# Kernel tuning notes

Measured on AMD Instinct MI355X. Metric: run time of the kernel, lower is better.

Reference implementation:

```python
import jax, jax.numpy as jnp
import numpy as np

B, T, D, H = 4, 1024, 1024, 16
DH = D // H
NEG_BIG = jnp.float32(-2.0**32 + 1)


def layer_norm(x, scale, bias, eps=1e-5):
    mean = jnp.mean(x, axis=-1, keepdims=True)
    var = jnp.mean(jnp.square(x - mean), axis=-1, keepdims=True)
    return (x - mean) * jax.lax.rsqrt(var + eps) * scale + bias


def setup_inputs() -> dict:
    key = jax.random.key(0)
    ks = jax.random.split(key, 10)
    s = 0.02
    x = jax.random.normal(ks[0], (B, T, D), jnp.float32)
    mask = jax.random.randint(ks[1], (B, T), 0, 2).astype(jnp.float32)
    return {
        "x": x,
        "mask": mask,
        "wq": jax.random.normal(ks[2], (D, D), jnp.float32) * s,
        "wk": jax.random.normal(ks[3], (D, D), jnp.float32) * s,
        "wv": jax.random.normal(ks[4], (D, D), jnp.float32) * s,
        "w1": jax.random.normal(ks[5], (D, D), jnp.float32) * s,
        "b1": jnp.zeros((D,), jnp.float32),
        "w2": jax.random.normal(ks[6], (D, D), jnp.float32) * s,
        "b2": jnp.zeros((D,), jnp.float32),
        "ln1_s": jnp.ones((D,), jnp.float32),
        "ln1_b": jnp.zeros((D,), jnp.float32),
        "ln2_s": jnp.ones((D,), jnp.float32),
        "ln2_b": jnp.zeros((D,), jnp.float32),
        "ln3_s": jnp.ones((D,), jnp.float32),
        "ln3_b": jnp.zeros((D,), jnp.float32),
    }


def _mask_enc(x, mask, wq, wk, wv, w1, b1, w2, b2,
              ln1_s, ln1_b, ln2_s, ln2_b, ln3_s, ln3_b):
    b, t, d = x.shape
    # --- multi-head attention (hand-rolled, matches torch split/cat trick) ---
    Q = (x @ wq).reshape(b, t, H, DH).transpose(0, 2, 1, 3)  # [B,H,T,dh]
    K = (x @ wk).reshape(b, t, H, DH).transpose(0, 2, 1, 3)
    V = (x @ wv).reshape(b, t, H, DH).transpose(0, 2, 1, 3)
    scores = jnp.einsum('bhqd,bhkd->bhqk', Q, K) / jnp.sqrt(jnp.float32(DH))
    # key padding mask from sign of |K| row sums
    key_m = jnp.sign(jnp.sum(jnp.abs(K), axis=-1))  # [B,H,T]
    scores = jnp.where(key_m[:, :, None, :] == 0, NEG_BIG, scores)
    # FORWARD direction: allowed where col_index > row_index (strict)
    idx = jnp.arange(t)
    allowed = (idx[None, :] > idx[:, None]).astype(scores.dtype)  # [T,T]
    scores = scores + (1.0 - allowed) * (-10000.0)
    attn = jax.nn.softmax(scores, axis=-1)
    # post-softmax query mask multiply
    query_m = jnp.sign(jnp.sum(jnp.abs(Q), axis=-1))[:, :, :, None]  # [B,H,T,1]
    attn = attn * query_m
    out = jnp.einsum('bhqk,bhkd->bhqd', attn, V)
    out = out.transpose(0, 2, 1, 3).reshape(b, t, d)  # combine heads
    out = out * mask[:, :, None]
    # --- residual + layernorm wrapper (attention) ---
    h1 = layer_norm(x + out, ln1_s, ln1_b)
    # --- FFN + residual + layernorm ---
    ffn = jax.nn.relu(h1 @ w1 + b1) @ w2 + b2
    h2 = layer_norm(h1 + ffn, ln2_s, ln2_b)
    # --- output normalization ---
    return layer_norm(h2, ln3_s, ln3_b)


def reference(x, mask, wq, wk, wv, w1, b1, w2, b2,
              ln1_s, ln1_b, ln2_s, ln2_b, ln3_s, ln3_b):
    return _mask_enc(x, mask, wq, wk, wv, w1, b1, w2, b2,
                     ln1_s, ln1_b, ln2_s, ln2_b, ln3_s, ln3_b)
```

## Files before the change

### kernel.cpp

```cpp
#include <hip/hip_runtime.h>
#include <stdint.h>


#define B_  4
#define T_  1024
#define D_  1024
#define H_  16
#define DH_ 64

typedef __attribute__((ext_vector_type(8))) short short8;
typedef __attribute__((ext_vector_type(4))) float floatx4;
typedef __attribute__((ext_vector_type(4))) _Float16 half4;

__device__ __forceinline__ unsigned short f2bf(float f) {
  union { float f; uint32_t u; } a; a.f = f;
  uint32_t r = a.u + 0x7FFFu + ((a.u >> 16) & 1u);
  return (unsigned short)(r >> 16);
}
__device__ __forceinline__ float bf2f(unsigned short u) {
  union { uint32_t u; float f; } a; a.u = ((uint32_t)u) << 16;
  return a.f;
}

#define GLD_LDS16(g, l) __builtin_amdgcn_global_load_lds( \
    (const __attribute__((address_space(1))) unsigned int*)(g), \
    (__attribute__((address_space(3))) unsigned int*)(l), 16, 0, 0)

__global__ __launch_bounds__(256)
void prep_kernel(const float4* __restrict__ x4, unsigned short* __restrict__ xb,
                 const float* __restrict__ w0, const float* __restrict__ w1,
                 const float* __restrict__ w2, const float* __restrict__ w3,
                 const float* __restrict__ w4, unsigned short* __restrict__ dst_all) {
  const int t = threadIdx.x;
  if (blockIdx.x < 1024) {
    int idx0 = blockIdx.x * 1024 + t;
#pragma unroll
    for (int c = 0; c < 4; ++c) {
      int idx = idx0 + c * 256;
      float4 v = x4[idx];
      union { uint2 u; unsigned short s[4]; } o;
      o.s[0] = f2bf(v.x); o.s[1] = f2bf(v.y); o.s[2] = f2bf(v.z); o.s[3] = f2bf(v.w);
      *(uint2*)&xb[(size_t)idx * 4] = o.u;
    }
    return;
  }
  const int b = blockIdx.x - 1024;
  const int z = b >> 8, ky = (b >> 4) & 15, nx = b & 15;
  const float* src = (z == 0) ? w0 : (z == 1) ? w1 : (z == 2) ? w2 : (z == 3) ? w3 : w4;
  unsigned short* dst = dst_all + (size_t)z * D_ * D_;
  __shared__ __align__(16) unsigned short tile[64 * 72];
  const int k0 = ky * 64, n0 = nx * 64;
#pragma unroll
  for (int c = 0; c < 4; ++c) {
    int idx = c * 256 + t;
    int r = idx >> 4, cc = (idx & 15) << 2;
    float4 v = *(const float4*)&src[(size_t)(k0 + r) * D_ + n0 + cc];
    tile[(cc + 0) * 72 + r] = f2bf(v.x);
    tile[(cc + 1) * 72 + r] = f2bf(v.y);
    tile[(cc + 2) * 72 + r] = f2bf(v.z);
    tile[(cc + 3) * 72 + r] = f2bf(v.w);
  }
  __syncthreads();
  int rr = t >> 2, ck = (t & 3) << 4;
  uint4 v0 = *(const uint4*)&tile[rr * 72 + ck];
  uint4 v1 = *(const uint4*)&tile[rr * 72 + ck + 8];
  *(uint4*)&dst[(size_t)(n0 + rr) * D_ + k0 + ck] = v0;
  *(uint4*)&dst[(size_t)(n0 + rr) * D_ + k0 + ck + 8] = v1;
}

__global__ __launch_bounds__(256, 2)
void gemm_qkv(const unsigned short* __restrict__ A,
              const unsigned short* __restrict__ Bt,
              unsigned short* __restrict__ oQ, unsigned short* __restrict__ oK,
              _Float16* __restrict__ oV) {
  const int K = 1024;
  __shared__ __align__(16) unsigned short As[128 * 32];
  __shared__ __align__(16) unsigned short Bs[128 * 32];
  __shared__ __align__(16) _Float16 Cs[2 * 64 * 136];
  const int t = threadIdx.x;
  const int lane = t & 63, w = t >> 6;
  const int quad = lane >> 4, lm = lane & 15;
  const int wm = w >> 1, wn = w & 1;
  const int m0 = blockIdx.y * 128, n0 = blockIdx.x * 128;
  const int arow = w * 32 + (lane >> 2), acol = (lane & 3) << 3;

  floatx4 acc[4][4];
#pragma unroll
  for (int i = 0; i < 4; ++i)
#pragma unroll
    for (int j = 0; j < 4; ++j) acc[i][j] = (floatx4){0.f, 0.f, 0.f, 0.f};

  for (int kt = 0; kt < K; kt += 32) {
    const unsigned short* ga = A + (size_t)(m0 + arow) * K + kt + acol;
    const unsigned short* gb = Bt + (size_t)(n0 + arow) * K + kt + acol;
    GLD_LDS16(ga, &As[(w * 32) * 32]);
    GLD_LDS16(ga + (size_t)16 * K, &As[(w * 32 + 16) * 32]);
    GLD_LDS16(gb, &Bs[(w * 32) * 32]);
    GLD_LDS16(gb + (size_t)16 * K, &Bs[(w * 32 + 16) * 32]);
    __syncthreads();
    short8 a[4], b[4];
#pragma unroll
    for (int i = 0; i < 4; ++i) a[i] = *(const short8*)&As[(wm * 64 + i * 16 + lm) * 32 + quad * 8];
#pragma unroll
    for (int j = 0; j < 4; ++j) b[j] = *(const short8*)&Bs[(wn * 64 + j * 16 + lm) * 32 + quad * 8];
#pragma unroll
    for (int i = 0; i < 4; ++i)
#pragma unroll
      for (int j = 0; j < 4; ++j)
        acc[i][j] = __builtin_amdgcn_mfma_f32_16x16x32_bf16(a[i], b[j], acc[i][j], 0, 0, 0);
    __syncthreads();
  }

  if (n0 < 2048) {
    unsigned short* p = (n0 < 1024) ? oQ : oK;
    const float qscale = (n0 < 1024) ? 0.18033688f : 1.0f;
#pragma unroll
    for (int i = 0; i < 4; ++i) {
      int gmb = m0 + wm * 64 + i * 16 + quad * 4;
#pragma unroll
      for (int j = 0; j < 4; ++j) {
        int gn = n0 + wn * 64 + j * 16 + lm;
        int nn = gn & 1023, hh = nn >> 6, dd = nn & 63;
#pragma unroll
        for (int r = 0; r < 4; ++r) {
          int gm = gmb + r;
          int bb = gm >> 10, tt = gm & 1023;
          p[(((size_t)bb * H_ + hh) * T_ + tt) * DH_ + dd] = f2bf(acc[i][j][r] * qscale);
        }
      }
    }
  } else {
#pragma unroll
    for (int i = 0; i < 4; ++i) {
#pragma unroll
      for (int j = 0; j < 4; ++j) {
        int gn = n0 + wn * 64 + j * 16 + lm;
        int hd = (gn >> 6) & 1, dd = gn & 63;
        int kperm = quad * 32 + (wm * 4 + i) * 4;
        union { _Float16 h[4]; uint2 u; } pk;
#pragma unroll
        for (int r = 0; r < 4; ++r) pk.h[r] = (_Float16)acc[i][j][r];
        *(uint2*)&Cs[((size_t)(hd * 64 + dd)) * 136 + kperm] = pk.u;
      }
    }
    __syncthreads();
    const int row = t >> 1, half = t & 1;
    const int hd = row >> 6, dd = row & 63;
    const int hh = ((n0 & 1023) >> 6) + hd;
    const int bb = m0 >> 10, kbg = (m0 >> 7) & 7;
    const _Float16* srcp = &Cs[(size_t)(hd * 64 + dd) * 136 + half * 64];
    _Float16* dstp = oV + ((((size_t)bb * H_ + hh) * DH_ + dd) * 8 + kbg) * 128 + half * 64;
#pragma unroll
    for (int g = 0; g < 8; ++g)
      *(uint4*)(dstp + g * 8) = *(const uint4*)(srcp + g * 8);
  }
}

template <int MODE>
__global__ __launch_bounds__(256, 2)
void gemm_ffn(const unsigned short* __restrict__ A,
              const unsigned short* __restrict__ Bt,
              unsigned short* __restrict__ oBf,
              const float* __restrict__ bias) {
  const int K = 1024, N = 1024;
  __shared__ __align__(16) unsigned short As[64 * 32];
  __shared__ __align__(16) unsigned short Bs[128 * 32];
  const int t = threadIdx.x;
  const int lane = t & 63, w = t >> 6;
  const int quad = lane >> 4, lm = lane & 15;
  const int wm = w >> 1, wn = w & 1;
  const int m0 = blockIdx.y * 64, n0 = blockIdx.x * 128;
  const int lrow = lane >> 2, lcol = (lane & 3) << 3;

  floatx4 acc[2][4];
#pragma unroll
  for (int i = 0; i < 2; ++i)
#pragma unroll
    for (int j = 0; j < 4; ++j) acc[i][j] = (floatx4){0.f, 0.f, 0.f, 0.f};

  for (int kt = 0; kt < K; kt += 32) {
    const unsigned short* ga = A + (size_t)(m0 + w * 16 + lrow) * K + kt + lcol;
    const unsigned short* gb = Bt + (size_t)(n0 + w * 32 + lrow) * K + kt + lcol;
    GLD_LDS16(ga, &As[(w * 16) * 32]);
    GLD_LDS16(gb, &Bs[(w * 32) * 32]);
    GLD_LDS16(gb + (size_t)16 * K, &Bs[(w * 32 + 16) * 32]);
    __syncthreads();
    short8 a[2], b[4];
#pragma unroll
    for (int i = 0; i < 2; ++i) a[i] = *(const short8*)&As[(wm * 32 + i * 16 + lm) * 32 + quad * 8];
#pragma unroll
    for (int j = 0; j < 4; ++j) b[j] = *(const short8*)&Bs[(wn * 64 + j * 16 + lm) * 32 + quad * 8];
#pragma unroll
    for (int i = 0; i < 2; ++i)
#pragma unroll
      for (int j = 0; j < 4; ++j)
        acc[i][j] = __builtin_amdgcn_mfma_f32_16x16x32_bf16(a[i], b[j], acc[i][j], 0, 0, 0);
    __syncthreads();
  }

#pragma unroll
  for (int i = 0; i < 2; ++i) {
    int gmb = m0 + wm * 32 + i * 16 + quad * 4;
#pragma unroll
    for (int j = 0; j < 4; ++j) {
      int gn = n0 + wn * 64 + j * 16 + lm;
      float bv = bias[gn];
#pragma unroll
      for (int r = 0; r < 4; ++r) {
        int gm = gmb + r;
        float v = acc[i][j][r] + bv;
        if (MODE == 1) v = fmaxf(v, 0.f);
        oBf[(size_t)gm * N + gn] = f2bf(v);
      }
    }
  }
}

__global__ __launch_bounds__(256)
void flash_attn(const unsigned short* __restrict__ Qb,
                const unsigned short* __restrict__ Kb,
                const _Float16* __restrict__ Vtg,
                const float* __restrict__ maskp,
                unsigned short* __restrict__ attn) {
  __shared__ __align__(16) unsigned short KLs[2][8192];
  __shared__ __align__(16) _Float16      VLs[2][8192];

  const int t = threadIdx.x;
  const int lane = t & 63, w = t >> 6;
  const int quad = lane >> 4, lm = lane & 15;

  const int bid = blockIdx.x;
  const int hi  = bid >> 8;
  const int lo  = bid & 255;
  const int xcd = lo & 7;
  const int hgrp = (lo >> 3) & 7;
  const int qpair = lo >> 6;
  const int qb = hi ? (7 - qpair) : qpair;
  const int head = hgrp * 8 + xcd;
  const int hh = head & 15, bb = head >> 4;
  const int q0 = qb << 7;

  const size_t headoff = ((size_t)bb * H_ + hh) * T_ * DH_;
  const unsigned short* Qh = Qb + headoff;
  const unsigned short* Kh = Kb + headoff;
  const _Float16* Vh = Vtg + headoff;

  short8 qf[2][2];
#pragma unroll
  for (int qg = 0; qg < 2; ++qg)
#pragma unroll
    for (int ks = 0; ks < 2; ++ks)
      qf[qg][ks] = *(const short8*)(Qh + (size_t)(q0 + w * 32 + qg * 16 + lm) * 64 + ks * 32 + quad * 8);

  float lsum[2] = {0.f, 0.f};
  floatx4 acc[2][4];
#pragma unroll
  for (int qg = 0; qg < 2; ++qg)
#pragma unroll
    for (int j2 = 0; j2 < 4; ++j2) acc[qg][j2] = (floatx4){0.f, 0.f, 0.f, 0.f};

  const int qglob0 = q0 + w * 32 + lm;
  const bool excl1 = (qglob0 + 16 == 1023);
  const float MSHIFT = 14426.950408f;

  const int my_lo  = (qb == 7 && w == 3) ? 0 : qb;
  const int blk_lo = (qb == 7) ? 0 : qb;

  const unsigned short* gk[4];
  const _Float16* gv[4];
#pragma unroll
  for (int i = 0; i < 4; ++i) {
    int s = w * 4 + i;
    gk[i] = Kh + (size_t)((s >> 1) * 16 + lm) * 64 + (s & 1) * 32 + quad * 8;
    gv[i] = Vh + ((size_t)((s >> 2) * 16 + lm) * 8) * 128 + quad * 32 + (s & 3) * 8;
  }

#pragma unroll
  for (int i = 0; i < 4; ++i) {
    int s = w * 4 + i;
    GLD_LDS16(gk[i] + (size_t)blk_lo * 8192, &KLs[0][s * 512]);
    GLD_LDS16(gv[i] + (size_t)blk_lo * 128,  &VLs[0][s * 512]);
  }

  int cur = 0;
  for (int kb = blk_lo; kb < 8; ++kb) {
    __syncthreads();
    if (kb + 1 < 8) {
      int nxt = cur ^ 1;
#pragma unroll
      for (int i = 0; i < 4; ++i) {
        int s = w * 4 + i;
        GLD_LDS16(gk[i] + (size_t)(kb + 1) * 8192, &KLs[nxt][s * 512]);
        GLD_LDS16(gv[i] + (size_t)(kb + 1) * 128,  &VLs[nxt][s * 512]);
      }
    }
    if (kb >= my_lo) {
      const unsigned short* Kc = &KLs[cur][0];
      const _Float16* Vc = &VLs[cur][0];
      const int k0 = kb * 128;
      const bool need_mask = (kb <= qb);

      short8 kA = *(const short8*)&Kc[(0 * 64 + lane) * 8];
      short8 kB = *(const short8*)&Kc[(1 * 64 + lane) * 8];
      half4 vA0 = *(const half4*)&Vc[((0 * 4 + 0) * 64 + lane) * 8];
      half4 vA1 = *(const half4*)&Vc[((1 * 4 + 0) * 64 + lane) * 8];
      half4 vA2 = *(const half4*)&Vc[((2 * 4 + 0) * 64 + lane) * 8];
      half4 vA3 = *(const half4*)&Vc[((3 * 4 + 0) * 64 + lane) * 8];

#pragma unroll
      for (int j = 0; j < 8; ++j) {
        short8 nA, nB; half4 n0, n1, n2, n3;
        if (j < 7) {
          int jn = j + 1;
          nA = *(const short8*)&Kc[((jn * 2 + 0) * 64 + lane) * 8];
          nB = *(const short8*)&Kc[((jn * 2 + 1) * 64 + lane) * 8];
          n0 = *(const half4*)&Vc[((0 * 4 + (jn >> 1)) * 64 + lane) * 8 + (jn & 1) * 4];
          n1 = *(const half4*)&Vc[((1 * 4 + (jn >> 1)) * 64 + lane) * 8 + (jn & 1) * 4];
          n2 = *(const half4*)&Vc[((2 * 4 + (jn >> 1)) * 64 + lane) * 8 + (jn & 1) * 4];
          n3 = *(const half4*)&Vc[((3 * 4 + (jn >> 1)) * 64 + lane) * 8 + (jn & 1) * 4];
        }
        floatx4 st[2];
#pragma unroll
        for (int qg = 0; qg < 2; ++qg) {
          floatx4 z = (floatx4){0.f, 0.f, 0.f, 0.f};
          z = __builtin_amdgcn_mfma_f32_16x16x32_bf16(kA, qf[qg][0], z, 0, 0, 0);
          st[qg] = __builtin_amdgcn_mfma_f32_16x16x32_bf16(kB, qf[qg][1], z, 0, 0, 0);
        }
        half4 pa[2];
#pragma unroll
        for (int qg = 0; qg < 2; ++qg) {
          const int qq = qglob0 + qg * 16;
          const bool skip = (qg == 1) && excl1;
#pragma unroll
          for (int r = 0; r < 4; ++r) {
            int kg = k0 + j * 16 + quad * 4 + r;
            float v = st[qg][r];
            if (need_mask && !skip && kg <= qq) v -= MSHIFT;
            float p = __builtin_amdgcn_exp2f(v);
            lsum[qg] += p;
            pa[qg][r] = (_Float16)p;
          }
        }
        acc[0][0] = __builtin_amdgcn_mfma_f32_16x16x16f16(pa[0], vA0, acc[0][0], 0, 0, 0);
        acc[1][0] = __builtin_amdgcn_mfma_f32_16x16x16f16(pa[1], vA0, acc[1][0], 0, 0, 0);
        acc[0][1] = __builtin_amdgcn_mfma_f32_16x16x16f16(pa[0], vA1, acc[0][1], 0, 0, 0);
        acc[1][1] = __builtin_amdgcn_mfma_f32_16x16x16f16(pa[1], vA1, acc[1][1], 0, 0, 0);
        acc[0][2] = __builtin_amdgcn_mfma_f32_16x16x16f16(pa[0], vA2, acc[0][2], 0, 0, 0);
        acc[1][2] = __builtin_amdgcn_mfma_f32_16x16x16f16(pa[1], vA2, acc[1][2], 0, 0, 0);
        acc[0][3] = __builtin_amdgcn_mfma_f32_16x16x16f16(pa[0], vA3, acc[0][3], 0, 0, 0);
        acc[1][3] = __builtin_amdgcn_mfma_f32_16x16x16f16(pa[1], vA3, acc[1][3], 0, 0, 0);
        kA = nA; kB = nB; vA0 = n0; vA1 = n1; vA2 = n2; vA3 = n3;
      }
    }
    cur ^= 1;
  }

#pragma unroll
  for (int qg = 0; qg < 2; ++qg) {
    float l = lsum[qg];
    l += __shfl_xor(l, 16);
    l += __shfl_xor(l, 32);
    float s = maskp[bb * T_ + qglob0 + qg * 16] / l;
#pragma unroll
    for (int r = 0; r < 4; ++r) {
      float bsc = __shfl(s, quad * 4 + r);
      int tq = q0 + w * 32 + qg * 16 + quad * 4 + r;
#pragma unroll
      for (int j2 = 0; j2 < 4; ++j2)
        attn[((size_t)(bb * T_ + tq)) * D_ + hh * 64 + j2 * 16 + lm] = f2bf(acc[qg][j2][r] * bsc);
    }
  }
}

__global__ __launch_bounds__(256)
void ln_res_kernel(const float* __restrict__ xa, const unsigned short* __restrict__ attn,
                   const float* __restrict__ sc, const float* __restrict__ bi,
                   float* __restrict__ h, unsigned short* __restrict__ hb) {
  const int t = threadIdx.x;
  const int lane = t & 63, w = t >> 6;
  const int row = blockIdx.x * 4 + w;
  const size_t base = (size_t)row * D_ + lane * 16;

  float v[16];
  float s1 = 0.f, s2 = 0.f;
#pragma unroll
  for (int i = 0; i < 4; ++i) {
    float4 a = *(const float4*)&xa[base + i * 4];
    union { uint2 u; unsigned short s[4]; } au;
    au.u = *(const uint2*)&attn[base + i * 4];
    float x0 = a.x + bf2f(au.s[0]);
    float x1 = a.y + bf2f(au.s[1]);
    float x2 = a.z + bf2f(au.s[2]);
    float x3 = a.w + bf2f(au.s[3]);
    v[i * 4 + 0] = x0; v[i * 4 + 1] = x1; v[i * 4 + 2] = x2; v[i * 4 + 3] = x3;
    s1 += x0 + x1 + x2 + x3;
    s2 += x0 * x0 + x1 * x1 + x2 * x2 + x3 * x3;
  }
#pragma unroll
  for (int off = 1; off < 64; off <<= 1) {
    s1 += __shfl_xor(s1, off);
    s2 += __shfl_xor(s2, off);
  }
  float mean = s1 * (1.f / 1024.f);
  float var = s2 * (1.f / 1024.f) - mean * mean;
  float rstd = rsqrtf(var + 1e-5f);
#pragma unroll
  for (int i = 0; i < 4; ++i) {
    float4 sv = *(const float4*)&sc[lane * 16 + i * 4];
    float4 bv = *(const float4*)&bi[lane * 16 + i * 4];
    float o0 = (v[i * 4 + 0] - mean) * rstd * sv.x + bv.x;
    float o1 = (v[i * 4 + 1] - mean) * rstd * sv.y + bv.y;
    float o2 = (v[i * 4 + 2] - mean) * rstd * sv.z + bv.z;
    float o3 = (v[i * 4 + 3] - mean) * rstd * sv.w + bv.w;
    float4 ov = {o0, o1, o2, o3};
    *(float4*)&h[base + i * 4] = ov;
    union { uint2 u; unsigned short s[4]; } ob;
    ob.s[0] = f2bf(o0); ob.s[1] = f2bf(o1); ob.s[2] = f2bf(o2); ob.s[3] = f2bf(o3);
    *(uint2*)&hb[base + i * 4] = ob.u;
  }
}

__global__ __launch_bounds__(256)
void ln_double_kernel(const float* __restrict__ h1, const unsigned short* __restrict__ ffnb,
                      const float* __restrict__ s2c, const float* __restrict__ b2c,
                      const float* __restrict__ s3c, const float* __restrict__ b3c,
                      float* __restrict__ out) {
  const int t = threadIdx.x;
  const int lane = t & 63, w = t >> 6;
  const int row = blockIdx.x * 4 + w;
  const size_t base = (size_t)row * D_ + lane * 16;

  float v[16];
  float s1 = 0.f, s2 = 0.f;
#pragma unroll
  for (int i = 0; i < 4; ++i) {
    float4 a = *(const float4*)&h1[base + i * 4];
    union { uint2 u; unsigned short s[4]; } fu;
    fu.u = *(const uint2*)&ffnb[base + i * 4];
    float x0 = a.x + bf2f(fu.s[0]);
    float x1 = a.y + bf2f(fu.s[1]);
    float x2 = a.z + bf2f(fu.s[2]);
    float x3 = a.w + bf2f(fu.s[3]);
    v[i * 4 + 0] = x0; v[i * 4 + 1] = x1; v[i * 4 + 2] = x2; v[i * 4 + 3] = x3;
    s1 += x0 + x1 + x2 + x3;
    s2 += x0 * x0 + x1 * x1 + x2 * x2 + x3 * x3;
  }
#pragma unroll
  for (int off = 1; off < 64; off <<= 1) {
    s1 += __shfl_xor(s1, off);
    s2 += __shfl_xor(s2, off);
  }
  float mean = s1 * (1.f / 1024.f);
  float var = s2 * (1.f / 1024.f) - mean * mean;
  float rstd = rsqrtf(var + 1e-5f);

  float o[16];
  float u1 = 0.f, u2 = 0.f;
#pragma unroll
  for (int i = 0; i < 4; ++i) {
    float4 sv = *(const float4*)&s2c[lane * 16 + i * 4];
    float4 bv = *(const float4*)&b2c[lane * 16 + i * 4];
    float o0 = (v[i * 4 + 0] - mean) * rstd * sv.x + bv.x;
    float o1 = (v[i * 4 + 1] - mean) * rstd * sv.y + bv.y;
    float o2 = (v[i * 4 + 2] - mean) * rstd * sv.z + bv.z;
    float o3 = (v[i * 4 + 3] - mean) * rstd * sv.w + bv.w;
    o[i * 4 + 0] = o0; o[i * 4 + 1] = o1; o[i * 4 + 2] = o2; o[i * 4 + 3] = o3;
    u1 += o0 + o1 + o2 + o3;
    u2 += o0 * o0 + o1 * o1 + o2 * o2 + o3 * o3;
  }
#pragma unroll
  for (int off = 1; off < 64; off <<= 1) {
    u1 += __shfl_xor(u1, off);
    u2 += __shfl_xor(u2, off);
  }
  float mean2 = u1 * (1.f / 1024.f);
  float var2 = u2 * (1.f / 1024.f) - mean2 * mean2;
  float rstd2 = rsqrtf(var2 + 1e-5f);
#pragma unroll
  for (int i = 0; i < 4; ++i) {
    float4 sv = *(const float4*)&s3c[lane * 16 + i * 4];
    float4 bv = *(const float4*)&b3c[lane * 16 + i * 4];
    float4 fo;
    fo.x = (o[i * 4 + 0] - mean2) * rstd2 * sv.x + bv.x;
    fo.y = (o[i * 4 + 1] - mean2) * rstd2 * sv.y + bv.y;
    fo.z = (o[i * 4 + 2] - mean2) * rstd2 * sv.z + bv.z;
    fo.w = (o[i * 4 + 3] - mean2) * rstd2 * sv.w + bv.w;
    *(float4*)&out[base + i * 4] = fo;
  }
}

extern "C" void kernel_launch(void* const* d_in, const int* in_sizes, int n_in,
                              void* d_out, int out_size, void* d_ws, size_t ws_size,
                              hipStream_t stream) {
  (void)in_sizes; (void)n_in; (void)out_size; (void)ws_size;
  const float* x   = (const float*)d_in[0];
  const float* msk = (const float*)d_in[1];
  const float* wq  = (const float*)d_in[2];
  const float* wk  = (const float*)d_in[3];
  const float* wv  = (const float*)d_in[4];
  const float* w1  = (const float*)d_in[5];
  const float* b1  = (const float*)d_in[6];
  const float* w2  = (const float*)d_in[7];
  const float* b2  = (const float*)d_in[8];
  const float* l1s = (const float*)d_in[9];
  const float* l1b = (const float*)d_in[10];
  const float* l2s = (const float*)d_in[11];
  const float* l2b = (const float*)d_in[12];
  const float* l3s = (const float*)d_in[13];
  const float* l3b = (const float*)d_in[14];
  float* outp = (float*)d_out;

  char* ws = (char*)d_ws;
  unsigned short* xb   = (unsigned short*)(ws);
  unsigned short* wt   = (unsigned short*)(ws + ((size_t)8  << 20));
  unsigned short* Qb   = (unsigned short*)(ws + ((size_t)18 << 20));
  unsigned short* Kb   = (unsigned short*)(ws + ((size_t)26 << 20));
  _Float16*       Vtg  = (_Float16*)(ws + ((size_t)34 << 20));
  unsigned short* attn = (unsigned short*)(ws + ((size_t)42 << 20));
  float* h1            = (float*)(ws + ((size_t)50 << 20));
  unsigned short* h1b  = (unsigned short*)(ws + ((size_t)18 << 20));
  unsigned short* gb   = (unsigned short*)(ws + ((size_t)26 << 20));
  unsigned short* ffnb = (unsigned short*)(ws + ((size_t)34 << 20));

  prep_kernel<<<1024 + 1280, 256, 0, stream>>>((const float4*)x, xb,
                                               wq, wk, wv, w1, w2, wt);
  gemm_qkv<<<dim3(24, 32), 256, 0, stream>>>(xb, wt, Qb, Kb, Vtg);
  flash_attn<<<512, 256, 0, stream>>>(Qb, Kb, Vtg, msk, attn);
  ln_res_kernel<<<1024, 256, 0, stream>>>(x, attn, l1s, l1b, h1, h1b);
  gemm_ffn<1><<<dim3(8, 64), 256, 0, stream>>>(h1b, wt + (size_t)3 * 1024 * 1024, gb, b1);
  gemm_ffn<2><<<dim3(8, 64), 256, 0, stream>>>(gb, wt + (size_t)4 * 1024 * 1024, ffnb, b2);
  ln_double_kernel<<<1024, 256, 0, stream>>>(h1, ffnb, l2s, l2b, l3s, l3b, outp);
}
```

Baseline: 236.4 us.

## Double GEMM K-tile to 64 with XOR-swizzled LDS layout in QKV and FFN GEMMs

Both the QKV and FFN GEMM kernels now stage 64-wide K slices per iteration instead of 32, which halves the number of barrier pairs per output tile. LDS rows are stored with an XOR swizzle of the 16-byte chunk index by row, to avoid bank conflicts on the MFMA fragment reads. In the QKV kernel, the staging buffers are overlaid with the epilogue C buffer in one raw shared array to keep LDS usage bounded. The FFN kernel's LDS footprint doubles, which may reduce occupancy.

```diff
diff --git a/kernel.cpp b/kernel.cpp
--- a/kernel.cpp
+++ b/kernel.cpp
@@ -74,15 +74,17 @@
               unsigned short* __restrict__ oQ, unsigned short* __restrict__ oK,
               _Float16* __restrict__ oV) {
   const int K = 1024;
-  __shared__ __align__(16) unsigned short As[128 * 32];
-  __shared__ __align__(16) unsigned short Bs[128 * 32];
-  __shared__ __align__(16) _Float16 Cs[2 * 64 * 136];
+  __shared__ __align__(16) unsigned char smem[34816];
+  unsigned short* As = (unsigned short*)smem;
+  unsigned short* Bs = (unsigned short*)(smem + 16384);
+  _Float16* Cs = (_Float16*)smem;
   const int t = threadIdx.x;
   const int lane = t & 63, w = t >> 6;
   const int quad = lane >> 4, lm = lane & 15;
   const int wm = w >> 1, wn = w & 1;
   const int m0 = blockIdx.y * 128, n0 = blockIdx.x * 128;
-  const int arow = w * 32 + (lane >> 2), acol = (lane & 3) << 3;
+  const int srow = lane >> 3;
+  const int scol = ((lane & 7) ^ srow) << 3;
 
   floatx4 acc[4][4];
 #pragma unroll
@@ -90,24 +92,29 @@
 #pragma unroll
     for (int j = 0; j < 4; ++j) acc[i][j] = (floatx4){0.f, 0.f, 0.f, 0.f};
 
-  for (int kt = 0; kt < K; kt += 32) {
-    const unsigned short* ga = A + (size_t)(m0 + arow) * K + kt + acol;
-    const unsigned short* gb = Bt + (size_t)(n0 + arow) * K + kt + acol;
-    GLD_LDS16(ga, &As[(w * 32) * 32]);
-    GLD_LDS16(ga + (size_t)16 * K, &As[(w * 32 + 16) * 32]);
-    GLD_LDS16(gb, &Bs[(w * 32) * 32]);
-    GLD_LDS16(gb + (size_t)16 * K, &Bs[(w * 32 + 16) * 32]);
+  for (int kt = 0; kt < K; kt += 64) {
+#pragma unroll
+    for (int i = 0; i < 4; ++i) {
+      const unsigned short* ga = A + (size_t)(m0 + w * 32 + i * 8 + srow) * K + kt + scol;
+      const unsigned short* gb = Bt + (size_t)(n0 + w * 32 + i * 8 + srow) * K + kt + scol;
+      GLD_LDS16(ga, &As[w * 2048 + i * 512]);
+      GLD_LDS16(gb, &Bs[w * 2048 + i * 512]);
+    }
     __syncthreads();
-    short8 a[4], b[4];
-#pragma unroll
-    for (int i = 0; i < 4; ++i) a[i] = *(const short8*)&As[(wm * 64 + i * 16 + lm) * 32 + quad * 8];
-#pragma unroll
-    for (int j = 0; j < 4; ++j) b[j] = *(const short8*)&Bs[(wn * 64 + j * 16 + lm) * 32 + quad * 8];
-#pragma unroll
-    for (int i = 0; i < 4; ++i)
-#pragma unroll
-      for (int j = 0; j < 4; ++j)
-        acc[i][j] = __builtin_amdgcn_mfma_f32_16x16x32_bf16(a[i], b[j], acc[i][j], 0, 0, 0);
+#pragma unroll
+    for (int ks = 0; ks < 2; ++ks) {
+      const int rs = ((ks * 4 + quad) ^ (lm & 7)) << 3;
+      short8 a[4], b[4];
+#pragma unroll
+      for (int i = 0; i < 4; ++i) a[i] = *(const short8*)&As[(wm * 64 + i * 16 + lm) * 64 + rs];
+#pragma unroll
+      for (int j = 0; j < 4; ++j) b[j] = *(const short8*)&Bs[(wn * 64 + j * 16 + lm) * 64 + rs];
+#pragma unroll
+      for (int i = 0; i < 4; ++i)
+#pragma unroll
+        for (int j = 0; j < 4; ++j)
+          acc[i][j] = __builtin_amdgcn_mfma_f32_16x16x32_bf16(a[i], b[j], acc[i][j], 0, 0, 0);
+    }
     __syncthreads();
   }
 
@@ -163,14 +170,15 @@
               unsigned short* __restrict__ oBf,
               const float* __restrict__ bias) {
   const int K = 1024, N = 1024;
-  __shared__ __align__(16) unsigned short As[64 * 32];
-  __shared__ __align__(16) unsigned short Bs[128 * 32];
+  __shared__ __align__(16) unsigned short As[64 * 64];
+  __shared__ __align__(16) unsigned short Bs[128 * 64];
   const int t = threadIdx.x;
   const int lane = t & 63, w = t >> 6;
   const int quad = lane >> 4, lm = lane & 15;
   const int wm = w >> 1, wn = w & 1;
   const int m0 = blockIdx.y * 64, n0 = blockIdx.x * 128;
-  const int lrow = lane >> 2, lcol = (lane & 3) << 3;
+  const int srow = lane >> 3;
+  const int scol = ((lane & 7) ^ srow) << 3;
 
   floatx4 acc[2][4];
 #pragma unroll
@@ -178,23 +186,32 @@
 #pragma unroll
     for (int j = 0; j < 4; ++j) acc[i][j] = (floatx4){0.f, 0.f, 0.f, 0.f};
 
-  for (int kt = 0; kt < K; kt += 32) {
-    const unsigned short* ga = A + (size_t)(m0 + w * 16 + lrow) * K + kt + lcol;
-    const unsigned short* gb = Bt + (size_t)(n0 + w * 32 + lrow) * K + kt + lcol;
-    GLD_LDS16(ga, &As[(w * 16) * 32]);
-    GLD_LDS16(gb, &Bs[(w * 32) * 32]);
-    GLD_LDS16(gb + (size_t)16 * K, &Bs[(w * 32 + 16) * 32]);
+  for (int kt = 0; kt < K; kt += 64) {
+#pragma unroll
+    for (int i = 0; i < 2; ++i) {
+      const unsigned short* ga = A + (size_t)(m0 + w * 16 + i * 8 + srow) * K + kt + scol;
+      GLD_LDS16(ga, &As[w * 1024 + i * 512]);
+    }
+#pragma unroll
+    for (int i = 0; i < 4; ++i) {
+      const unsigned short* gb = Bt + (size_t)(n0 + w * 32 + i * 8 + srow) * K + kt + scol;
+      GLD_LDS16(gb, &Bs[w * 2048 + i * 512]);
+    }
     __syncthreads();
-    short8 a[2], b[4];
-#pragma unroll
-    for (int i = 0; i < 2; ++i) a[i] = *(const short8*)&As[(wm * 32 + i * 16 + lm) * 32 + quad * 8];
-#pragma unroll
-    for (int j = 0; j < 4; ++j) b[j] = *(const short8*)&Bs[(wn * 64 + j * 16 + lm) * 32 + quad * 8];
-#pragma unroll
-    for (int i = 0; i < 2; ++i)
-#pragma unroll
-      for (int j = 0; j < 4; ++j)
-        acc[i][j] = __builtin_amdgcn_mfma_f32_16x16x32_bf16(a[i], b[j], acc[i][j], 0, 0, 0);
+#pragma unroll
+    for (int ks = 0; ks < 2; ++ks) {
+      const int rs = ((ks * 4 + quad) ^ (lm & 7)) << 3;
+      short8 a[2], b[4];
+#pragma unroll
+      for (int i = 0; i < 2; ++i) a[i] = *(const short8*)&As[(wm * 32 + i * 16 + lm) * 64 + rs];
+#pragma unroll
+      for (int j = 0; j < 4; ++j) b[j] = *(const short8*)&Bs[(wn * 64 + j * 16 + lm) * 64 + rs];
+#pragma unroll
+      for (int i = 0; i < 2; ++i)
+#pragma unroll
+        for (int j = 0; j < 4; ++j)
+          acc[i][j] = __builtin_amdgcn_mfma_f32_16x16x32_bf16(a[i], b[j], acc[i][j], 0, 0, 0);
+    }
     __syncthreads();
   }
 
```

Result: faster. 228.0 us (-3.5%).
